# Optimization experiments

Measured on AMD Instinct MI355X. Metric: run time of the kernel, lower is better.

Reference implementation:

```python
import jax, jax.numpy as jnp
import numpy as np

VOCAB, EMBED, HID = 32000, 512, 1024
B, S = 64, 512


def setup_inputs() -> dict:
    key = jax.random.key(0)
    ks = jax.random.split(key, 14)
    sc = lambda fan: 1.0 / np.sqrt(fan)
    return {
        "input_token": jax.random.randint(ks[0], (B, 1), 0, VOCAB),
        "h": jax.random.normal(ks[1], (1, B, HID), jnp.float32),
        "c": jax.random.normal(ks[2], (1, B, HID), jnp.float32),
        "encoder_outputs": jax.random.normal(ks[3], (B, S, HID), jnp.float32),
        "emb": jax.random.normal(ks[4], (VOCAB, EMBED), jnp.float32).at[0].set(0.0),
        "W1": jax.random.normal(ks[5], (HID, HID), jnp.float32) * sc(HID),
        "W2": jax.random.normal(ks[6], (HID, HID), jnp.float32) * sc(HID),
        "v": jax.random.normal(ks[7], (HID,), jnp.float32) * sc(HID),
        "W_ih": jax.random.normal(ks[8], (4 * HID, EMBED + HID), jnp.float32) * sc(EMBED + HID),
        "W_hh": jax.random.normal(ks[9], (4 * HID, HID), jnp.float32) * sc(HID),
        "b_ih": jax.random.normal(ks[10], (4 * HID,), jnp.float32) * 0.01,
        "b_hh": jax.random.normal(ks[11], (4 * HID,), jnp.float32) * 0.01,
        "fc_W": jax.random.normal(ks[12], (VOCAB, 2 * HID), jnp.float32) * sc(2 * HID),
        "fc_b": jax.random.normal(ks[13], (VOCAB,), jnp.float32) * 0.01,
    }


def reference(input_token, h, c, encoder_outputs, emb, W1, W2, v,
              W_ih, W_hh, b_ih, b_hh, fc_W, fc_b):
    # Embedding (dropout = identity in eval)
    embedded = emb[input_token[:, 0]]                       # [B, E]
    h0 = h[0]                                               # [B, H]
    c0 = c[0]                                               # [B, H]

    # Bahdanau additive attention
    dh = h0 @ W1.T                                          # [B, H]
    eh = jnp.einsum('bsh,kh->bsk', encoder_outputs, W2)     # [B, S, H]
    energy = jnp.tanh(dh[:, None, :] + eh)                  # [B, S, H]
    scores = jnp.einsum('bsh,h->bs', energy, v)             # [B, S]
    attn = jax.nn.softmax(scores, axis=-1)                  # [B, S]
    context = jnp.einsum('bs,bsh->bh', attn, encoder_outputs)  # [B, H]

    # Single LSTM step (PyTorch gate order: i, f, g, o)
    x = jnp.concatenate([embedded, context], axis=-1)       # [B, E+H]
    gates = x @ W_ih.T + b_ih + h0 @ W_hh.T + b_hh          # [B, 4H]
    i, f, g, o = jnp.split(gates, 4, axis=-1)
    c1 = jax.nn.sigmoid(f) * c0 + jax.nn.sigmoid(i) * jnp.tanh(g)
    h1 = jax.nn.sigmoid(o) * jnp.tanh(c1)                   # [B, H]

    # Output projection
    out = jnp.concatenate([h1, context], axis=-1)           # [B, 2H]
    prediction = out @ fc_W.T + fc_b                        # [B, V]
    return prediction, (h1[None], c1[None]), attn
```

## Files before the change

### kernel.cpp

```cpp
#include <hip/hip_runtime.h>
#include <math.h>

#define VOCAB 32000
#define EMBED 512
#define HID   1024
#define BATCH 64
#define SEQ   512

#define OUT_H1   2048000
#define OUT_C1   2113536
#define OUT_ATTN 2179072

typedef __bf16 bf16x8 __attribute__((ext_vector_type(8)));
typedef float  f32x4  __attribute__((ext_vector_type(4)));

__device__ __forceinline__ unsigned short f2bf(float f) {
  unsigned int u = __builtin_bit_cast(unsigned int, f);
  u += 0x7fffu + ((u >> 16) & 1u);
  return (unsigned short)(u >> 16);
}
__device__ __forceinline__ float bf2f(unsigned int u) {
  return __builtin_bit_cast(float, u << 16);
}

__device__ __forceinline__ float fast_tanh(float x) {
  float cx = fminf(fmaxf(x, -15.f), 15.f);
  float t = __builtin_amdgcn_exp2f(cx * 2.8853900817779268f);
  return (t - 1.f) / (t + 1.f);
}

__device__ __forceinline__ void gload16(const unsigned short* g, unsigned short* l) {
  __builtin_amdgcn_global_load_lds(
      (const __attribute__((address_space(1))) void*)g,
      (__attribute__((address_space(3))) void*)l, 16, 0, 0);
}

__global__ void f2bf_kernel(const float* __restrict__ src, unsigned short* __restrict__ dst,
                            int n8) {
  int i = blockIdx.x * blockDim.x + threadIdx.x;
  int stride = gridDim.x * blockDim.x;
  for (; i < n8; i += stride) {
    const float* s = src + (size_t)i * 8;
    float4 f0 = *(const float4*)s;
    float4 f1 = *(const float4*)(s + 4);
    union { unsigned short us[8]; uint4 u; } p;
    p.us[0]=f2bf(f0.x); p.us[1]=f2bf(f0.y); p.us[2]=f2bf(f0.z); p.us[3]=f2bf(f0.w);
    p.us[4]=f2bf(f1.x); p.us[5]=f2bf(f1.y); p.us[6]=f2bf(f1.z); p.us[7]=f2bf(f1.w);
    *(uint4*)(dst + (size_t)i * 8) = p.u;
  }
}

__global__ void dh_w2_kernel(const float* __restrict__ h0, const float* __restrict__ W1,
                             float* __restrict__ dh,
                             const float* __restrict__ W2, unsigned short* __restrict__ W2b) {
  __shared__ float hs[HID];
  int bid = blockIdx.x, t = threadIdx.x;
  if (bid < 256) {
    int b = bid >> 2, kblk = bid & 3;
    for (int i = t; i < HID; i += 256) hs[i] = h0[b * HID + i];
    __syncthreads();
    int k = kblk * 256 + t;
    const float* w = W1 + (size_t)k * HID;
    float acc = 0.f;
    for (int hh = 0; hh < HID; hh += 4) {
      float4 wv = *(const float4*)(w + hh);
      float4 hv = *(const float4*)(hs + hh);
      acc += wv.x * hv.x + wv.y * hv.y + wv.z * hv.z + wv.w * hv.w;
    }
    dh[b * HID + k] = acc;
  } else {
    int i = (bid - 256) * 256 + t;
    const float* s = W2 + (size_t)i * 8;
    float4 f0 = *(const float4*)s;
    float4 f1 = *(const float4*)(s + 4);
    union { unsigned short us[8]; uint4 u; } p;
    p.us[0]=f2bf(f0.x); p.us[1]=f2bf(f0.y); p.us[2]=f2bf(f0.z); p.us[3]=f2bf(f0.w);
    p.us[4]=f2bf(f1.x); p.us[5]=f2bf(f1.y); p.us[6]=f2bf(f1.z); p.us[7]=f2bf(f1.w);
    *(uint4*)(W2b + (size_t)i * 8) = p.u;
  }
}

__launch_bounds__(512, 2)
__global__ void scores8_kernel(const unsigned short* __restrict__ encb,
                               const unsigned short* __restrict__ W2b,
                               const float* __restrict__ dh, const float* __restrict__ v,
                               float* __restrict__ spart) {
  __shared__ __align__(16) unsigned short sA[2][16384];
  __shared__ __align__(16) unsigned short sB[2][16384];
  __shared__ float dh_s[256];
  __shared__ float v_s[256];
  __shared__ float red4[4][256];

  int bid = blockIdx.x;
  int wg = (bid & 7) * 64 + (bid >> 3);
  int mt = wg >> 2, nt = wg & 3;
  int m0 = mt * 256, n0 = nt * 256;

  int t = threadIdx.x;
  int wid = t >> 6, l = t & 63;
  int wr = wid >> 2, wc = wid & 3;
  int fr = l & 15, co = (l >> 4) * 8;

  const unsigned short* pa0;
  const unsigned short* pb0;
  int do0 = wid * 512;
  {
    int row0 = wid * 8 + (l >> 3);
    int colE = ((l & 7) ^ ((l >> 3) & 7)) << 3;
    pa0 = encb + (size_t)(m0 + row0) * HID + colE;
    pb0 = W2b + (size_t)(n0 + row0) * HID + colE;
  }

  f32x4 acc[8][4];
#pragma unroll
  for (int i = 0; i < 8; i++)
#pragma unroll
    for (int j = 0; j < 4; j++) acc[i][j] = (f32x4){0.f, 0.f, 0.f, 0.f};

#define SC_STAGE(T, d)                                                         \
  do {                                                                         \
    int k0_ = (T) * 64;                                                        \
    gload16(pa0 + k0_,          &sA[d][do0]);                                  \
    gload16(pa0 + 65536 + k0_,  &sA[d][do0 + 4096]);                           \
    gload16(pa0 + 131072 + k0_, &sA[d][do0 + 8192]);                           \
    gload16(pa0 + 196608 + k0_, &sA[d][do0 + 12288]);                          \
    gload16(pb0 + k0_,          &sB[d][do0]);                                  \
    gload16(pb0 + 65536 + k0_,  &sB[d][do0 + 4096]);                           \
    gload16(pb0 + 131072 + k0_, &sB[d][do0 + 8192]);                           \
    gload16(pb0 + 196608 + k0_, &sB[d][do0 + 12288]);                          \
  } while (0)

  SC_STAGE(0, 0);
  SC_STAGE(1, 1);

#define LDF(Mat, row, ks) \
  (*(const bf16x8*)&Mat[(row) * 64 + (((ks) * 32 + co) ^ (((row) & 7) << 3))])

  for (int T = 0; T < 16; ++T) {
    int d = T & 1;
    if (T == 15) asm volatile("s_waitcnt vmcnt(0)" ::: "memory");
    else         asm volatile("s_waitcnt vmcnt(8)" ::: "memory");
    asm volatile("s_barrier" ::: "memory");
    const unsigned short* A = sA[d];
    const unsigned short* B = sB[d];
    bf16x8 a[4][2], b[4][2];
#pragma unroll
    for (int jj = 0; jj < 4; ++jj)
#pragma unroll
      for (int ks = 0; ks < 2; ++ks)
        b[jj][ks] = LDF(B, wc * 64 + jj * 16 + fr, ks);
#pragma unroll
    for (int ii = 0; ii < 4; ++ii)
#pragma unroll
      for (int ks = 0; ks < 2; ++ks)
        a[ii][ks] = LDF(A, wr * 128 + ii * 16 + fr, ks);
    __builtin_amdgcn_s_setprio(1);
#pragma unroll
    for (int ii = 0; ii < 4; ++ii)
#pragma unroll
      for (int jj = 0; jj < 2; ++jj)
#pragma unroll
        for (int ks = 0; ks < 2; ++ks)
          acc[ii][jj] = __builtin_amdgcn_mfma_f32_16x16x32_bf16(a[ii][ks], b[jj][ks], acc[ii][jj], 0, 0, 0);
    __builtin_amdgcn_s_setprio(0);
    __builtin_amdgcn_s_setprio(1);
#pragma unroll
    for (int ii = 0; ii < 4; ++ii)
#pragma unroll
      for (int jj = 2; jj < 4; ++jj)
#pragma unroll
        for (int ks = 0; ks < 2; ++ks)
          acc[ii][jj] = __builtin_amdgcn_mfma_f32_16x16x32_bf16(a[ii][ks], b[jj][ks], acc[ii][jj], 0, 0, 0);
    __builtin_amdgcn_s_setprio(0);
#pragma unroll
    for (int ii = 0; ii < 4; ++ii)
#pragma unroll
      for (int ks = 0; ks < 2; ++ks)
        a[ii][ks] = LDF(A, wr * 128 + 64 + ii * 16 + fr, ks);
    __builtin_amdgcn_s_setprio(1);
#pragma unroll
    for (int ii = 0; ii < 4; ++ii)
#pragma unroll
      for (int jj = 2; jj < 4; ++jj)
#pragma unroll
        for (int ks = 0; ks < 2; ++ks)
          acc[4 + ii][jj] = __builtin_amdgcn_mfma_f32_16x16x32_bf16(a[ii][ks], b[jj][ks], acc[4 + ii][jj], 0, 0, 0);
    __builtin_amdgcn_s_setprio(0);
    __builtin_amdgcn_s_setprio(1);
#pragma unroll
    for (int ii = 0; ii < 4; ++ii)
#pragma unroll
      for (int jj = 0; jj < 2; ++jj)
#pragma unroll
        for (int ks = 0; ks < 2; ++ks)
          acc[4 + ii][jj] = __builtin_amdgcn_mfma_f32_16x16x32_bf16(a[ii][ks], b[jj][ks], acc[4 + ii][jj], 0, 0, 0);
    __builtin_amdgcn_s_setprio(0);
    asm volatile("s_barrier" ::: "memory");
    if (T < 14) SC_STAGE(T + 2, d);
  }
#undef LDF
#undef SC_STAGE

  int b = m0 >> 9;
  if (t < 256) { dh_s[t] = dh[b * HID + n0 + t]; v_s[t] = v[n0 + t]; }
  __syncthreads();
  float sp[32];
#pragma unroll
  for (int q = 0; q < 32; ++q) sp[q] = 0.f;
#pragma unroll
  for (int ii = 0; ii < 8; ++ii)
#pragma unroll
    for (int jj = 0; jj < 4; ++jj) {
      int nl = wc * 64 + jj * 16 + fr;
      float dv = dh_s[nl], vv = v_s[nl];
#pragma unroll
      for (int r = 0; r < 4; ++r)
        sp[ii * 4 + r] += fast_tanh(dv + acc[ii][jj][r]) * vv;
    }
#pragma unroll
  for (int q = 0; q < 32; ++q) {
    float x = sp[q];
    x += __shfl_xor(x, 1);
    x += __shfl_xor(x, 2);
    x += __shfl_xor(x, 4);
    x += __shfl_xor(x, 8);
    sp[q] = x;
  }
  if (fr == 0) {
    int rl = wr * 128 + (l >> 4) * 4;
#pragma unroll
    for (int ii = 0; ii < 8; ++ii)
#pragma unroll
      for (int r = 0; r < 4; ++r)
        red4[wc][rl + ii * 16 + r] = sp[ii * 4 + r];
  }
  __syncthreads();
  if (t < 256)
    spart[nt * 32768 + m0 + t] = red4[0][t] + red4[1][t] + red4[2][t] + red4[3][t];
}

__global__ void softmax_kernel(const float* __restrict__ spart, float* __restrict__ attn,
                               float* __restrict__ ctx) {
  __shared__ float red[8];
  int b = blockIdx.x, t = threadIdx.x;
  int row = b * SEQ + t;
  float x = spart[row] + spart[32768 + row] + spart[65536 + row] + spart[98304 + row];
  float m = x;
  for (int d = 1; d < 64; d <<= 1) m = fmaxf(m, __shfl_xor(m, d));
  if ((t & 63) == 0) red[t >> 6] = m;
  __syncthreads();
  float bm = red[0];
#pragma unroll
  for (int i = 1; i < 8; i++) bm = fmaxf(bm, red[i]);
  float e = expf(x - bm);
  float s = e;
  for (int d = 1; d < 64; d <<= 1) s += __shfl_xor(s, d);
  __syncthreads();
  if ((t & 63) == 0) red[t >> 6] = s;
  __syncthreads();
  float bs = 0.f;
#pragma unroll
  for (int i = 0; i < 8; i++) bs += red[i];
  attn[b * SEQ + t] = e / bs;
  ctx[b * HID + t] = 0.f;
  ctx[b * HID + 512 + t] = 0.f;
}

__global__ void context2_kernel(const unsigned short* __restrict__ encb,
                                const float* __restrict__ attn, float* __restrict__ ctx) {
  __shared__ float a_s[64];
  int b = blockIdx.y, s0 = blockIdx.x * 64, t = threadIdx.x;
  if (t < 64) a_s[t] = attn[b * SEQ + s0 + t];
  __syncthreads();
  int hg = (t & 127) * 8, sg = (t >> 7) * 32;
  float a0 = 0.f, a1 = 0.f, a2 = 0.f, a3 = 0.f, a4 = 0.f, a5 = 0.f, a6 = 0.f, a7 = 0.f;
  const unsigned short* base = encb + ((size_t)b * SEQ + s0 + sg) * HID + hg;
  for (int s = 0; s < 32; s++) {
    uint4 ev = *(const uint4*)(base + (size_t)s * HID);
    float a = a_s[sg + s];
    a0 += a * bf2f(ev.x & 0xffffu); a1 += a * bf2f(ev.x >> 16);
    a2 += a * bf2f(ev.y & 0xffffu); a3 += a * bf2f(ev.y >> 16);
    a4 += a * bf2f(ev.z & 0xffffu); a5 += a * bf2f(ev.z >> 16);
    a6 += a * bf2f(ev.w & 0xffffu); a7 += a * bf2f(ev.w >> 16);
  }
  atomicAdd(&ctx[b * HID + hg + 0], a0);
  atomicAdd(&ctx[b * HID + hg + 1], a1);
  atomicAdd(&ctx[b * HID + hg + 2], a2);
  atomicAdd(&ctx[b * HID + hg + 3], a3);
  atomicAdd(&ctx[b * HID + hg + 4], a4);
  atomicAdd(&ctx[b * HID + hg + 5], a5);
  atomicAdd(&ctx[b * HID + hg + 6], a6);
  atomicAdd(&ctx[b * HID + hg + 7], a7);
}

__launch_bounds__(256)
__global__ void gates8p_kernel(const int* __restrict__ tok, const float* __restrict__ emb,
                               const float* __restrict__ ctx, const float* __restrict__ h0,
                               const float* __restrict__ W_ih, const float* __restrict__ W_hh,
                               float* __restrict__ gpart) {
  __shared__ __align__(16) unsigned short lA[64 * 40];
  __shared__ __align__(16) unsigned short lB[128 * 40];
  int n0 = blockIdx.x * 128, kz = blockIdx.y;
  int kbase = kz * 320;
  int t = threadIdx.x, w = t >> 6, l = t & 63;
  f32x4 acc[4][2];
#pragma unroll
  for (int i = 0; i < 4; i++)
#pragma unroll
    for (int j = 0; j < 2; j++) acc[i][j] = (f32x4){0.f, 0.f, 0.f, 0.f};
  int rowA = t >> 2, qA = (t & 3) * 8;
  int rowB = t >> 1, hB = t & 1;
  int tkA = tok[rowA];

  for (int kt = 0; kt < 10; kt++) {
    int k0 = kbase + kt * 32;
    {
      int kg = k0 + qA;
      const float* src;
      if (kg < 512)        src = emb + (size_t)tkA * EMBED + kg;
      else if (kg < 1536)  src = ctx + rowA * HID + (kg - 512);
      else                 src = h0 + rowA * HID + (kg - 1536);
      float4 f0 = *(const float4*)src;
      float4 f1 = *(const float4*)(src + 4);
      union { unsigned short us[8]; uint4 u; } p;
      p.us[0]=f2bf(f0.x); p.us[1]=f2bf(f0.y); p.us[2]=f2bf(f0.z); p.us[3]=f2bf(f0.w);
      p.us[4]=f2bf(f1.x); p.us[5]=f2bf(f1.y); p.us[6]=f2bf(f1.z); p.us[7]=f2bf(f1.w);
      *(uint4*)&lA[rowA * 40 + qA] = p.u;
    }
    {
      int kg = k0 + hB * 16;
      const float* src = (kg < 1536) ? (W_ih + (size_t)(n0 + rowB) * 1536 + kg)
                                     : (W_hh + (size_t)(n0 + rowB) * 1024 + (kg - 1536));
      float4 f0 = *(const float4*)src;
      float4 f1 = *(const float4*)(src + 4);
      float4 f2 = *(const float4*)(src + 8);
      float4 f3 = *(const float4*)(src + 12);
      union { unsigned short us[16]; uint4 u4[2]; } p;
      p.us[0]=f2bf(f0.x);  p.us[1]=f2bf(f0.y);  p.us[2]=f2bf(f0.z);  p.us[3]=f2bf(f0.w);
      p.us[4]=f2bf(f1.x);  p.us[5]=f2bf(f1.y);  p.us[6]=f2bf(f1.z);  p.us[7]=f2bf(f1.w);
      p.us[8]=f2bf(f2.x);  p.us[9]=f2bf(f2.y);  p.us[10]=f2bf(f2.z); p.us[11]=f2bf(f2.w);
      p.us[12]=f2bf(f3.x); p.us[13]=f2bf(f3.y); p.us[14]=f2bf(f3.z); p.us[15]=f2bf(f3.w);
      *(uint4*)&lB[rowB * 40 + hB * 16 + 0] = p.u4[0];
      *(uint4*)&lB[rowB * 40 + hB * 16 + 8] = p.u4[1];
    }
    __syncthreads();
    bf16x8 af[4], bv[2];
    int co = (l >> 4) * 8;
#pragma unroll
    for (int i = 0; i < 4; i++) af[i] = *(const bf16x8*)&lA[(i * 16 + (l & 15)) * 40 + co];
#pragma unroll
    for (int j = 0; j < 2; j++) bv[j] = *(const bf16x8*)&lB[(w * 32 + j * 16 + (l & 15)) * 40 + co];
#pragma unroll
    for (int i = 0; i < 4; i++)
#pragma unroll
      for (int j = 0; j < 2; j++)
        acc[i][j] = __builtin_amdgcn_mfma_f32_16x16x32_bf16(af[i], bv[j], acc[i][j], 0, 0, 0);
    __syncthreads();
  }
#pragma unroll
  for (int i = 0; i < 4; i++)
#pragma unroll
    for (int j = 0; j < 2; j++) {
      int n = n0 + w * 32 + j * 16 + (l & 15);
#pragma unroll
      for (int r = 0; r < 4; r++) {
        int m = i * 16 + (l >> 4) * 4 + r;
        gpart[(size_t)kz * 262144 + (size_t)m * 4096 + n] = acc[i][j][r];
      }
    }
}

__global__ void lstm_kernel(const float* __restrict__ gpart, const float* __restrict__ b_ih,
                            const float* __restrict__ b_hh, const float* __restrict__ c0,
                            float* __restrict__ out) {
  int b = blockIdx.y;
  int hh = blockIdx.x * 256 + threadIdx.x;
  float gi = b_ih[hh]        + b_hh[hh];
  float gf = b_ih[1024 + hh] + b_hh[1024 + hh];
  float gg = b_ih[2048 + hh] + b_hh[2048 + hh];
  float go = b_ih[3072 + hh] + b_hh[3072 + hh];
#pragma unroll
  for (int kz = 0; kz < 8; kz++) {
    const float* g = gpart + (size_t)kz * 262144 + (size_t)b * 4096;
    gi += g[hh];
    gf += g[1024 + hh];
    gg += g[2048 + hh];
    go += g[3072 + hh];
  }
  float si = 1.f / (1.f + expf(-gi));
  float sf = 1.f / (1.f + expf(-gf));
  float so = 1.f / (1.f + expf(-go));
  float c1 = sf * c0[b * HID + hh] + si * tanhf(gg);
  float h1 = so * tanhf(c1);
  out[OUT_H1 + b * HID + hh] = h1;
  out[OUT_C1 + b * HID + hh] = c1;
}

__launch_bounds__(256)
__global__ void fc64_kernel(const float* __restrict__ h1, const float* __restrict__ ctx,
                            const float* __restrict__ fcW, float* __restrict__ part) {
  __shared__ __align__(16) unsigned short lA[64 * 40];
  __shared__ __align__(16) unsigned short lB[64 * 40];
  int n0 = blockIdx.x * 64, kz = blockIdx.y;
  const float* A = kz ? ctx : h1;
  int t = threadIdx.x, w = t >> 6, l = t & 63;
  int fr = l & 15;
  f32x4 acc[4];
#pragma unroll
  for (int i = 0; i < 4; i++) acc[i] = (f32x4){0.f, 0.f, 0.f, 0.f};
  int rowS = t >> 2, qS = (t & 3) * 8;

  for (int kt = 0; kt < 32; kt++) {
    int k0 = kt * 32;
    {
      const float* src = A + rowS * HID + k0 + qS;
      float4 f0 = *(const float4*)src;
      float4 f1 = *(const float4*)(src + 4);
      union { unsigned short us[8]; uint4 u; } p;
      p.us[0]=f2bf(f0.x); p.us[1]=f2bf(f0.y); p.us[2]=f2bf(f0.z); p.us[3]=f2bf(f0.w);
      p.us[4]=f2bf(f1.x); p.us[5]=f2bf(f1.y); p.us[6]=f2bf(f1.z); p.us[7]=f2bf(f1.w);
      *(uint4*)&lA[rowS * 40 + qS] = p.u;
    }
    {
      const float* src = fcW + (size_t)(n0 + rowS) * 2048 + kz * 1024 + k0 + qS;
      float4 f0 = *(const float4*)src;
      float4 f1 = *(const float4*)(src + 4);
      union { unsigned short us[8]; uint4 u; } p;
      p.us[0]=f2bf(f0.x); p.us[1]=f2bf(f0.y); p.us[2]=f2bf(f0.z); p.us[3]=f2bf(f0.w);
      p.us[4]=f2bf(f1.x); p.us[5]=f2bf(f1.y); p.us[6]=f2bf(f1.z); p.us[7]=f2bf(f1.w);
      *(uint4*)&lB[rowS * 40 + qS] = p.u;
    }
    __syncthreads();
    bf16x8 af[4], bv;
    int co = (l >> 4) * 8;
#pragma unroll
    for (int i = 0; i < 4; i++) af[i] = *(const bf16x8*)&lA[(i * 16 + fr) * 40 + co];
    bv = *(const bf16x8*)&lB[(w * 16 + fr) * 40 + co];
#pragma unroll
    for (int i = 0; i < 4; i++)
      acc[i] = __builtin_amdgcn_mfma_f32_16x16x32_bf16(af[i], bv, acc[i], 0, 0, 0);
    __syncthreads();
  }
#pragma unroll
  for (int i = 0; i < 4; i++) {
    int n = n0 + w * 16 + fr;
#pragma unroll
    for (int r = 0; r < 4; r++) {
      int m = i * 16 + (l >> 4) * 4 + r;
      part[(size_t)kz * 2048000 + (size_t)m * VOCAB + n] = acc[i][r];
    }
  }
}

__global__ void fc_combine_kernel(const float* __restrict__ part,
                                  const float* __restrict__ fcb, float* __restrict__ pred) {
  int i = blockIdx.x * 256 + threadIdx.x;
  int m = i / 8000, n4 = i % 8000;
  size_t e = (size_t)m * VOCAB + n4 * 4;
  float4 p0 = *(const float4*)(part + e);
  float4 p1 = *(const float4*)(part + 2048000 + e);
  float4 bb = *(const float4*)(fcb + n4 * 4);
  float4 o;
  o.x = p0.x + p1.x + bb.x;
  o.y = p0.y + p1.y + bb.y;
  o.z = p0.z + p1.z + bb.z;
  o.w = p0.w + p1.w + bb.w;
  *(float4*)(pred + e) = o;
}

extern "C" void kernel_launch(void* const* d_in, const int* in_sizes, int n_in,
                              void* d_out, int out_size, void* d_ws, size_t ws_size,
                              hipStream_t stream) {
  const int*   tok  = (const int*)d_in[0];
  const float* h    = (const float*)d_in[1];
  const float* c    = (const float*)d_in[2];
  const float* enc  = (const float*)d_in[3];
  const float* emb  = (const float*)d_in[4];
  const float* W1   = (const float*)d_in[5];
  const float* W2   = (const float*)d_in[6];
  const float* v    = (const float*)d_in[7];
  const float* W_ih = (const float*)d_in[8];
  const float* W_hh = (const float*)d_in[9];
  const float* b_ih = (const float*)d_in[10];
  const float* b_hh = (const float*)d_in[11];
  const float* fcW  = (const float*)d_in[12];
  const float* fcb  = (const float*)d_in[13];
  float* out = (float*)d_out;

  float* wsf    = (float*)d_ws;
  float* spart  = wsf;
  float* ctx    = wsf + 131072;
  float* dh     = wsf + 196608;
  float* gpart  = wsf + 262144;
  float* part   = wsf + 2359296;
  unsigned short* encb = (unsigned short*)(wsf + 6455296);
  unsigned short* W2b  = encb + (size_t)BATCH * SEQ * HID;

  f2bf_kernel<<<2048, 256, 0, stream>>>(enc, encb, BATCH * SEQ * HID / 8);
  dh_w2_kernel<<<768, 256, 0, stream>>>(h, W1, dh, W2, W2b);
  scores8_kernel<<<512, 512, 0, stream>>>(encb, W2b, dh, v, spart);
  softmax_kernel<<<64, 512, 0, stream>>>(spart, out + OUT_ATTN, ctx);
  context2_kernel<<<dim3(8, 64), 256, 0, stream>>>(encb, out + OUT_ATTN, ctx);
  gates8p_kernel<<<dim3(32, 8), 256, 0, stream>>>(tok, emb, ctx, h, W_ih, W_hh, gpart);
  lstm_kernel<<<dim3(4, 64), 256, 0, stream>>>(gpart, b_ih, b_hh, c, out);
  fc64_kernel<<<dim3(500, 2), 256, 0, stream>>>(out + OUT_H1, ctx, fcW, part);
  fc_combine_kernel<<<2000, 256, 0, stream>>>(part, fcb, out);
}
```

Baseline: 271.2 us.

## Fuse FC split-K halves and bias into a single full-K kernel

The output projection previously ran as a two-way split-K over the h1 and context halves, wrote 2x64x32000 fp32 partials, and then added them with bias in a separate combine kernel. Each block now walks the full K=2048 with 512 threads and 64-wide K tiles, adds the bias in the epilogue and writes the prediction directly. This removes the partial-sum writes and reads (about 16 MB of traffic) plus one launch. In exchange the grid halves to 500 blocks, which lowers parallelism for the fcW streaming load.

Result: faster. 263.1 us (-3.0%).

```diff
diff --git a/kernel.cpp b/kernel.cpp
--- a/kernel.cpp
+++ b/kernel.cpp
@@ -396,76 +396,64 @@
   out[OUT_C1 + b * HID + hh] = c1;
 }
 
-__launch_bounds__(256)
-__global__ void fc64_kernel(const float* __restrict__ h1, const float* __restrict__ ctx,
-                            const float* __restrict__ fcW, float* __restrict__ part) {
-  __shared__ __align__(16) unsigned short lA[64 * 40];
-  __shared__ __align__(16) unsigned short lB[64 * 40];
-  int n0 = blockIdx.x * 64, kz = blockIdx.y;
-  const float* A = kz ? ctx : h1;
+__launch_bounds__(512)
+__global__ void fcK2048_kernel(const float* __restrict__ h1, const float* __restrict__ ctx,
+                               const float* __restrict__ fcW, const float* __restrict__ fcb,
+                               float* __restrict__ pred) {
+  __shared__ __align__(16) unsigned short lA[64 * 72];
+  __shared__ __align__(16) unsigned short lB[64 * 72];
+  int n0 = blockIdx.x * 64;
   int t = threadIdx.x, w = t >> 6, l = t & 63;
-  int fr = l & 15;
-  f32x4 acc[4];
-#pragma unroll
-  for (int i = 0; i < 4; i++) acc[i] = (f32x4){0.f, 0.f, 0.f, 0.f};
-  int rowS = t >> 2, qS = (t & 3) * 8;
+  int wr = w >> 2, wc = w & 3;
+  int fr = l & 15, co = (l >> 4) * 8;
+  f32x4 acc[2];
+  acc[0] = (f32x4){0.f, 0.f, 0.f, 0.f};
+  acc[1] = (f32x4){0.f, 0.f, 0.f, 0.f};
+  int rowS = t >> 3, qS = (t & 7) * 8;
 
   for (int kt = 0; kt < 32; kt++) {
-    int k0 = kt * 32;
+    int k0 = kt * 64;
     {
-      const float* src = A + rowS * HID + k0 + qS;
+      int kg = k0 + qS;
+      const float* src = (kg < 1024) ? (h1 + rowS * HID + kg) : (ctx + rowS * HID + kg - 1024);
       float4 f0 = *(const float4*)src;
       float4 f1 = *(const float4*)(src + 4);
       union { unsigned short us[8]; uint4 u; } p;
       p.us[0]=f2bf(f0.x); p.us[1]=f2bf(f0.y); p.us[2]=f2bf(f0.z); p.us[3]=f2bf(f0.w);
       p.us[4]=f2bf(f1.x); p.us[5]=f2bf(f1.y); p.us[6]=f2bf(f1.z); p.us[7]=f2bf(f1.w);
-      *(uint4*)&lA[rowS * 40 + qS] = p.u;
+      *(uint4*)&lA[rowS * 72 + qS] = p.u;
     }
     {
-      const float* src = fcW + (size_t)(n0 + rowS) * 2048 + kz * 1024 + k0 + qS;
+      const float* src = fcW + (size_t)(n0 + rowS) * 2048 + k0 + qS;
       float4 f0 = *(const float4*)src;
       float4 f1 = *(const float4*)(src + 4);
       union { unsigned short us[8]; uint4 u; } p;
       p.us[0]=f2bf(f0.x); p.us[1]=f2bf(f0.y); p.us[2]=f2bf(f0.z); p.us[3]=f2bf(f0.w);
       p.us[4]=f2bf(f1.x); p.us[5]=f2bf(f1.y); p.us[6]=f2bf(f1.z); p.us[7]=f2bf(f1.w);
-      *(uint4*)&lB[rowS * 40 + qS] = p.u;
+      *(uint4*)&lB[rowS * 72 + qS] = p.u;
     }
     __syncthreads();
-    bf16x8 af[4], bv;
-    int co = (l >> 4) * 8;
-#pragma unroll
-    for (int i = 0; i < 4; i++) af[i] = *(const bf16x8*)&lA[(i * 16 + fr) * 40 + co];
-    bv = *(const bf16x8*)&lB[(w * 16 + fr) * 40 + co];
-#pragma unroll
-    for (int i = 0; i < 4; i++)
-      acc[i] = __builtin_amdgcn_mfma_f32_16x16x32_bf16(af[i], bv, acc[i], 0, 0, 0);
+    bf16x8 a0, a1, bv;
+#pragma unroll
+    for (int ks = 0; ks < 2; ks++) {
+      a0 = *(const bf16x8*)&lA[(wr * 32 + fr) * 72 + ks * 32 + co];
+      a1 = *(const bf16x8*)&lA[(wr * 32 + 16 + fr) * 72 + ks * 32 + co];
+      bv = *(const bf16x8*)&lB[(wc * 16 + fr) * 72 + ks * 32 + co];
+      acc[0] = __builtin_amdgcn_mfma_f32_16x16x32_bf16(a0, bv, acc[0], 0, 0, 0);
+      acc[1] = __builtin_amdgcn_mfma_f32_16x16x32_bf16(a1, bv, acc[1], 0, 0, 0);
+    }
     __syncthreads();
   }
-#pragma unroll
-  for (int i = 0; i < 4; i++) {
-    int n = n0 + w * 16 + fr;
+  int n = n0 + wc * 16 + fr;
+  float bias = fcb[n];
+#pragma unroll
+  for (int i = 0; i < 2; i++) {
 #pragma unroll
     for (int r = 0; r < 4; r++) {
-      int m = i * 16 + (l >> 4) * 4 + r;
-      part[(size_t)kz * 2048000 + (size_t)m * VOCAB + n] = acc[i][r];
-    }
-  }
-}
-
-__global__ void fc_combine_kernel(const float* __restrict__ part,
-                                  const float* __restrict__ fcb, float* __restrict__ pred) {
-  int i = blockIdx.x * 256 + threadIdx.x;
-  int m = i / 8000, n4 = i % 8000;
-  size_t e = (size_t)m * VOCAB + n4 * 4;
-  float4 p0 = *(const float4*)(part + e);
-  float4 p1 = *(const float4*)(part + 2048000 + e);
-  float4 bb = *(const float4*)(fcb + n4 * 4);
-  float4 o;
-  o.x = p0.x + p1.x + bb.x;
-  o.y = p0.y + p1.y + bb.y;
-  o.z = p0.z + p1.z + bb.z;
-  o.w = p0.w + p1.w + bb.w;
-  *(float4*)(pred + e) = o;
+      int m = wr * 32 + i * 16 + (l >> 4) * 4 + r;
+      pred[(size_t)m * VOCAB + n] = acc[i][r] + bias;
+    }
+  }
 }
 
 extern "C" void kernel_launch(void* const* d_in, const int* in_sizes, int n_in,
@@ -492,8 +480,7 @@
   float* ctx    = wsf + 131072;
   float* dh     = wsf + 196608;
   float* gpart  = wsf + 262144;
-  float* part   = wsf + 2359296;
-  unsigned short* encb = (unsigned short*)(wsf + 6455296);
+  unsigned short* encb = (unsigned short*)(wsf + 2359296);
   unsigned short* W2b  = encb + (size_t)BATCH * SEQ * HID;
 
   f2bf_kernel<<<2048, 256, 0, stream>>>(enc, encb, BATCH * SEQ * HID / 8);
@@ -503,6 +490,5 @@
   context2_kernel<<<dim3(8, 64), 256, 0, stream>>>(encb, out + OUT_ATTN, ctx);
   gates8p_kernel<<<dim3(32, 8), 256, 0, stream>>>(tok, emb, ctx, h, W_ih, W_hh, gpart);
   lstm_kernel<<<dim3(4, 64), 256, 0, stream>>>(gpart, b_ih, b_hh, c, out);
-  fc64_kernel<<<dim3(500, 2), 256, 0, stream>>>(out + OUT_H1, ctx, fcW, part);
-  fc_combine_kernel<<<2000, 256, 0, stream>>>(part, fcb, out);
-}
+  fcK2048_kernel<<<500, 512, 0, stream>>>(out + OUT_H1, ctx, fcW, fcb, out);
+}
```
